# Performance work log

Hardware: AMD Instinct MI355X
Metric: run time of the kernel (lower is better)

The kernel has to match this reference:

```python
import jax, jax.numpy as jnp
import numpy as np

L, N, D = 4, 50000, 64        # lookback, n_nodes, gnn_dim
E = 500000                    # n_edges
HID = 256
LN_EPS = 1e-5


def setup_inputs() -> dict:
    key = jax.random.key(0)
    ks = jax.random.split(key, 8)
    h_all = jax.random.normal(ks[0], (L, N, D), dtype=jnp.float32)
    src = jax.random.randint(ks[1], (E,), 0, N, dtype=jnp.int32)
    dst = jax.random.randint(ks[2], (E,), 0, N, dtype=jnp.int32)
    W1 = jax.random.normal(ks[3], (HID, L * 2 * D), dtype=jnp.float32) * (1.0 / np.sqrt(L * 2 * D))
    b1 = jax.random.normal(ks[4], (HID,), dtype=jnp.float32) * 0.01
    W3 = jax.random.normal(ks[5], (1, HID), dtype=jnp.float32) * (1.0 / np.sqrt(HID))
    b3 = jax.random.normal(ks[6], (1,), dtype=jnp.float32) * 0.01
    gamma2 = jnp.ones((HID,), dtype=jnp.float32)
    beta2 = jnp.zeros((HID,), dtype=jnp.float32)
    return {"h_all": h_all, "src": src, "dst": dst, "W1": W1, "b1": b1,
            "W3": W3, "b3": b3, "gamma2": gamma2, "beta2": beta2}


def reference(h_all, src, dst, W1, b1, W3, b3, gamma2, beta2):
    lb, _, d = h_all.shape
    # importance weights 1..L normalized
    imp = jnp.arange(1, lb + 1, dtype=h_all.dtype)
    imp = imp / imp.sum()
    # per-edge gather of src/dst features for every lookback step: [L, E, 2D]
    hs = h_all[:, src]                                  # [L, E, D]
    hd = h_all[:, dst]                                  # [L, E, D]
    embed = jnp.concatenate([hs, hd], axis=-1) * imp[:, None, None]
    # concat over lookback steps -> [E, L*2D]
    embed = jnp.transpose(embed, (1, 0, 2)).reshape(embed.shape[1], -1)
    # MLP: W1(tanh) -> LayerNorm -> dropout(eval=identity) -> relu -> W3
    x = jnp.tanh(embed) @ W1.T + b1                     # [E, HID]
    mu = jnp.mean(x, axis=-1, keepdims=True)
    var = jnp.var(x, axis=-1, keepdims=True)
    x = (x - mu) * jax.lax.rsqrt(var + LN_EPS) * gamma2 + beta2
    x = jax.nn.relu(x)
    out = x @ W3.T + b3                                 # [E, 1]
    return out[:, 0]
```

## Files before the change

kernel.cpp:

```cpp
#include <hip/hip_runtime.h>
#include <hip/hip_bf16.h>

#define LL 4
#define NN 50000
#define DD 64
#define EE 500000
#define HID 256
#define KDIM 512
#define LN_EPS 1e-5f

typedef __bf16 bf16x8 __attribute__((ext_vector_type(8)));
typedef float f32x16 __attribute__((ext_vector_type(16)));

__device__ __forceinline__ void async16(const void* g, void* l) {
    __builtin_amdgcn_global_load_lds(
        (const __attribute__((address_space(1))) void*)g,
        (__attribute__((address_space(3))) void*)l, 16, 0, 0);
}

__global__ void tanh_conv(const float* __restrict__ h, __bf16* __restrict__ t) {
    int i = (blockIdx.x * 256 + threadIdx.x) * 8;
    int l = i / (NN * DD);
    float imp = (float)(l + 1) * 0.1f;
    const float4* p = (const float4*)(h + i);
    float4 a = p[0];
    float4 b = p[1];
    float x[8] = {a.x, a.y, a.z, a.w, b.x, b.y, b.z, b.w};
    bf16x8 r;
    #pragma unroll
    for (int j = 0; j < 8; ++j) {
        float e2 = __expf(2.0f * (imp * x[j]));
        r[j] = (__bf16)(1.0f - 2.0f / (e2 + 1.0f));
    }
    *(bf16x8*)(t + i) = r;
}

__global__ void w2_conv(const float* __restrict__ w1, __bf16* __restrict__ o) {
    int t = blockIdx.x * 256 + threadIdx.x;
    int j  = t & 511;
    int b  = t >> 9;
    int k0 = (b >> 1) * 16 + (b & 1) * 8;
    int r  = j & 255;
    int col = (k0 >> 6) * 128 + ((j >> 8) ? 64 : 0) + (k0 & 63);
    const float4* p = (const float4*)(w1 + r * KDIM + col);
    float4 va = p[0];
    float4 vb = p[1];
    bf16x8 v;
    v[0] = (__bf16)va.x; v[1] = (__bf16)va.y; v[2] = (__bf16)va.z; v[3] = (__bf16)va.w;
    v[4] = (__bf16)vb.x; v[5] = (__bf16)vb.y; v[6] = (__bf16)vb.z; v[7] = (__bf16)vb.w;
    *(bf16x8*)(o + (size_t)t * 8) = v;
}

__global__ __launch_bounds__(256, 2)
void node_proj(const __bf16* __restrict__ tb, const __bf16* __restrict__ w2c,
               const float* __restrict__ b1, __bf16* __restrict__ P) {
    __shared__ __align__(16) char smem[65536];
    __bf16* Bs = (__bf16*)smem;
    float*  Cs = (float*)smem;

    const int tid  = threadIdx.x;
    const int wave = tid >> 6;
    const int lane = tid & 63;
    const int h32  = lane >> 5;
    const int c32  = lane & 31;
    const int cb   = blockIdx.y;
    const int n00  = blockIdx.x * 128;

    #pragma unroll
    for (int it = 0; it < 16; ++it) {
        int o = it * 2048 + tid * 8;
        async16(w2c + (size_t)(o >> 10) * 4096 + cb * 1024 + (o & 1023), Bs + o);
    }

    int node = n00 + wave * 32 + c32;
    if (node >= NN) node = NN - 1;
    uint4 a[16];
    #pragma unroll
    for (int u = 0; u < 16; ++u) {
        const __bf16* p = tb + (size_t)(u >> 2) * (NN * DD) + node * DD
                        + (u & 3) * 16 + h32 * 8;
        a[u] = *(const uint4*)p;
    }

    f32x16 acc[4];
    #pragma unroll
    for (int nt = 0; nt < 4; ++nt) acc[nt] = (f32x16)(0.f);

    __syncthreads();

    #pragma unroll
    for (int u = 0; u < 16; ++u) {
        bf16x8 af = __builtin_bit_cast(bf16x8, a[u]);
        const __bf16* Bk = Bs + (u * 2 + h32) * 1024 + c32 * 8;
        #pragma unroll
        for (int nt = 0; nt < 4; ++nt) {
            bf16x8 bf = *(const bf16x8*)(Bk + nt * 256);
            acc[nt] = __builtin_amdgcn_mfma_f32_32x32x16_bf16(af, bf, acc[nt], 0, 0, 0);
        }
    }
    __syncthreads();

    #pragma unroll
    for (int nt = 0; nt < 4; ++nt) {
        #pragma unroll
        for (int r = 0; r < 16; ++r) {
            int nl = wave * 32 + (r & 3) + 8 * (r >> 2) + 4 * h32;
            Cs[nl * 128 + nt * 32 + c32] = acc[nt][r];
        }
    }
    __syncthreads();
    #pragma unroll
    for (int it = 0; it < 8; ++it) {
        int o  = it * 2048 + tid * 8;
        int nl = o >> 7;
        int n  = n00 + nl;
        if (n < NN) {
            int hbase = ((cb & 1) << 7) | (o & 127);
            bf16x8 v;
            #pragma unroll
            for (int z = 0; z < 8; ++z)
                v[z] = (__bf16)(Cs[o + z] + 0.5f * b1[hbase + z]);
            *(bf16x8*)(P + (size_t)n * 512 + cb * 128 + (o & 127)) = v;
        }
    }
}

__global__ __launch_bounds__(256, 5)
void edge_out(const __bf16* __restrict__ P, const int* __restrict__ src,
              const int* __restrict__ dst, const float* __restrict__ w3,
              const float* __restrict__ b3, const float* __restrict__ gamma,
              const float* __restrict__ beta, float* __restrict__ out) {
    const int tid = threadIdx.x;
    const int g   = tid >> 4;
    const int j   = tid & 15;
    const int lb  = (g & 3) << 4;

    float gv[16], btv[16], wv[16];
    {
        const float4* pg = (const float4*)(gamma + j * 16);
        const float4* pt = (const float4*)(beta + j * 16);
        const float4* pw = (const float4*)(w3 + j * 16);
        #pragma unroll
        for (int z = 0; z < 4; ++z) {
            float4 vg = pg[z], vt = pt[z], vw = pw[z];
            gv [z*4+0] = vg.x; gv [z*4+1] = vg.y; gv [z*4+2] = vg.z; gv [z*4+3] = vg.w;
            btv[z*4+0] = vt.x; btv[z*4+1] = vt.y; btv[z*4+2] = vt.z; btv[z*4+3] = vt.w;
            wv [z*4+0] = vw.x; wv [z*4+1] = vw.y; wv [z*4+2] = vw.z; wv [z*4+3] = vw.w;
        }
    }
    const float b3v = b3[0];
    const int e0 = blockIdx.x * 128 + g * 8;

    int ej = e0 + (j & 7);
    if (ej >= EE) ej = EE - 1;
    const int sv = src[ej];
    const int dv = dst[ej];

    #pragma unroll
    for (int i = 0; i < 8; ++i) {
        const int s = __shfl(sv, lb + i);
        const int d = __shfl(dv, lb + i);
        const uint4* ps = (const uint4*)(P + ((size_t)s << 9) + (j << 4));
        const uint4* pd = (const uint4*)(P + ((size_t)d << 9) + 256 + (j << 4));
        uint4 rs0 = ps[0], rs1 = ps[1];
        uint4 rd0 = pd[0], rd1 = pd[1];
        bf16x8 A0 = __builtin_bit_cast(bf16x8, rs0);
        bf16x8 A1 = __builtin_bit_cast(bf16x8, rs1);
        bf16x8 C0 = __builtin_bit_cast(bf16x8, rd0);
        bf16x8 C1 = __builtin_bit_cast(bf16x8, rd1);
        float x[16];
        #pragma unroll
        for (int z = 0; z < 8; ++z) {
            x[z]     = (float)A0[z] + (float)C0[z];
            x[z + 8] = (float)A1[z] + (float)C1[z];
        }
        float sum = 0.f, sq = 0.f;
        #pragma unroll
        for (int z = 0; z < 16; ++z) {
            sum += x[z];
            sq   = fmaf(x[z], x[z], sq);
        }
        #pragma unroll
        for (int m = 1; m < 16; m <<= 1) {
            sum += __shfl_xor(sum, m);
            sq  += __shfl_xor(sq,  m);
        }
        float mu = sum * (1.0f / 256.0f);
        float rs = rsqrtf(sq * (1.0f / 256.0f) - mu * mu + LN_EPS);
        float dot = 0.f;
        #pragma unroll
        for (int z = 0; z < 16; ++z) {
            float t = (x[z] - mu) * rs;
            float y = fmaxf(fmaf(t, gv[z], btv[z]), 0.f);
            dot = fmaf(y, wv[z], dot);
        }
        #pragma unroll
        for (int m = 1; m < 16; m <<= 1) dot += __shfl_xor(dot, m);
        int e = e0 + i;
        if (j == 0 && e < EE) out[e] = dot + b3v;
    }
}

extern "C" void kernel_launch(void* const* d_in, const int* in_sizes, int n_in,
                              void* d_out, int out_size, void* d_ws, size_t ws_size,
                              hipStream_t stream) {
    const float* h_all  = (const float*)d_in[0];
    const int*   src    = (const int*)  d_in[1];
    const int*   dst    = (const int*)  d_in[2];
    const float* W1     = (const float*)d_in[3];
    const float* b1     = (const float*)d_in[4];
    const float* W3     = (const float*)d_in[5];
    const float* b3     = (const float*)d_in[6];
    const float* gamma2 = (const float*)d_in[7];
    const float* beta2  = (const float*)d_in[8];
    float* out = (float*)d_out;

    __bf16* tb  = (__bf16*)d_ws;
    __bf16* w2c = tb + (size_t)LL * NN * DD;
    __bf16* P   = w2c + 131072;

    tanh_conv<<<6250, 256, 0, stream>>>(h_all, tb);
    w2_conv<<<64, 256, 0, stream>>>(W1, w2c);
    node_proj<<<dim3((NN + 127) / 128, 4), 256, 0, stream>>>(tb, w2c, b1, P);
    edge_out<<<(EE + 127) / 128, 256, 0, stream>>>(P, src, dst, W3, b3,
                                                   gamma2, beta2, out);
}
```

Before: 211.3 us.

## Halve node_proj tile width and software-pipeline edge gathers in edge_out

```diff
diff --git a/kernel.cpp b/kernel.cpp
--- a/kernel.cpp
+++ b/kernel.cpp
@@ -51,10 +51,10 @@
     *(bf16x8*)(o + (size_t)t * 8) = v;
 }
 
-__global__ __launch_bounds__(256, 2)
+__global__ __launch_bounds__(256, 4)
 void node_proj(const __bf16* __restrict__ tb, const __bf16* __restrict__ w2c,
                const float* __restrict__ b1, __bf16* __restrict__ P) {
-    __shared__ __align__(16) char smem[65536];
+    __shared__ __align__(16) char smem[32768];
     __bf16* Bs = (__bf16*)smem;
     float*  Cs = (float*)smem;
 
@@ -66,12 +66,6 @@
     const int cb   = blockIdx.y;
     const int n00  = blockIdx.x * 128;
 
-    #pragma unroll
-    for (int it = 0; it < 16; ++it) {
-        int o = it * 2048 + tid * 8;
-        async16(w2c + (size_t)(o >> 10) * 4096 + cb * 1024 + (o & 1023), Bs + o);
-    }
-
     int node = n00 + wave * 32 + c32;
     if (node >= NN) node = NN - 1;
     uint4 a[16];
@@ -82,66 +76,118 @@
         a[u] = *(const uint4*)p;
     }
 
-    f32x16 acc[4];
-    #pragma unroll
-    for (int nt = 0; nt < 4; ++nt) acc[nt] = (f32x16)(0.f);
+    #pragma unroll
+    for (int it = 0; it < 8; ++it) {
+        int o = it * 2048 + tid * 8;
+        async16(w2c + (size_t)(o >> 9) * 4096 + cb * 512 + (o & 511), Bs + o);
+    }
+
+    f32x16 acc[2];
+    acc[0] = (f32x16)(0.f);
+    acc[1] = (f32x16)(0.f);
 
     __syncthreads();
 
     #pragma unroll
     for (int u = 0; u < 16; ++u) {
         bf16x8 af = __builtin_bit_cast(bf16x8, a[u]);
-        const __bf16* Bk = Bs + (u * 2 + h32) * 1024 + c32 * 8;
-        #pragma unroll
-        for (int nt = 0; nt < 4; ++nt) {
-            bf16x8 bf = *(const bf16x8*)(Bk + nt * 256);
-            acc[nt] = __builtin_amdgcn_mfma_f32_32x32x16_bf16(af, bf, acc[nt], 0, 0, 0);
-        }
+        const __bf16* Bk = Bs + (u * 2 + h32) * 512 + c32 * 8;
+        acc[0] = __builtin_amdgcn_mfma_f32_32x32x16_bf16(
+            af, *(const bf16x8*)(Bk), acc[0], 0, 0, 0);
+        acc[1] = __builtin_amdgcn_mfma_f32_32x32x16_bf16(
+            af, *(const bf16x8*)(Bk + 256), acc[1], 0, 0, 0);
     }
     __syncthreads();
 
     #pragma unroll
-    for (int nt = 0; nt < 4; ++nt) {
+    for (int nt = 0; nt < 2; ++nt) {
         #pragma unroll
         for (int r = 0; r < 16; ++r) {
             int nl = wave * 32 + (r & 3) + 8 * (r >> 2) + 4 * h32;
-            Cs[nl * 128 + nt * 32 + c32] = acc[nt][r];
+            Cs[nl * 64 + nt * 32 + c32] = acc[nt][r];
         }
     }
     __syncthreads();
     #pragma unroll
-    for (int it = 0; it < 8; ++it) {
-        int o  = it * 2048 + tid * 8;
-        int nl = o >> 7;
-        int n  = n00 + nl;
+    for (int it = 0; it < 4; ++it) {
+        int o   = it * 2048 + tid * 8;
+        int nl  = o >> 6;
+        int col = o & 63;
+        int n   = n00 + nl;
         if (n < NN) {
-            int hbase = ((cb & 1) << 7) | (o & 127);
+            int hbase = (cb & 3) * 64 + col;
             bf16x8 v;
             #pragma unroll
             for (int z = 0; z < 8; ++z)
                 v[z] = (__bf16)(Cs[o + z] + 0.5f * b1[hbase + z]);
-            *(bf16x8*)(P + (size_t)n * 512 + cb * 128 + (o & 127)) = v;
+            *(bf16x8*)(P + (size_t)n * 512 + cb * 64 + col) = v;
         }
     }
 }
 
-__global__ __launch_bounds__(256, 5)
+#define LOADB(R)                                                              \
+    do {                                                                      \
+        _Pragma("unroll")                                                     \
+        for (int t = 0; t < 4; ++t) {                                         \
+            int s = __shfl(sv, lb + eb + t);                                  \
+            int d = __shfl(dv, lb + eb + t);                                  \
+            R##0[t] = *(const uint4*)(P + ((size_t)s << 9) + (j << 3));       \
+            R##1[t] = *(const uint4*)(P + ((size_t)d << 9) + 256 + (j << 3)); \
+        }                                                                     \
+    } while (0)
+
+#define COMPB(R, B)                                                           \
+    do {                                                                      \
+        _Pragma("unroll")                                                     \
+        for (int t = 0; t < 4; ++t) {                                         \
+            bf16x8 A = __builtin_bit_cast(bf16x8, R##0[t]);                   \
+            bf16x8 C = __builtin_bit_cast(bf16x8, R##1[t]);                   \
+            float x[8];                                                       \
+            _Pragma("unroll")                                                 \
+            for (int z = 0; z < 8; ++z) x[z] = (float)A[z] + (float)C[z];     \
+            float sum = 0.f, sq = 0.f;                                        \
+            _Pragma("unroll")                                                 \
+            for (int z = 0; z < 8; ++z) {                                     \
+                sum += x[z];                                                  \
+                sq   = fmaf(x[z], x[z], sq);                                  \
+            }                                                                 \
+            _Pragma("unroll")                                                 \
+            for (int m = 1; m < 32; m <<= 1) {                                \
+                sum += __shfl_xor(sum, m);                                    \
+                sq  += __shfl_xor(sq,  m);                                    \
+            }                                                                 \
+            float mu = sum * (1.0f / 256.0f);                                 \
+            float rs = rsqrtf(sq * (1.0f / 256.0f) - mu * mu + LN_EPS);       \
+            float dot = 0.f;                                                  \
+            _Pragma("unroll")                                                 \
+            for (int z = 0; z < 8; ++z) {                                     \
+                float y = fmaxf(fmaf((x[z] - mu) * rs, gv[z], btv[z]), 0.f);  \
+                dot = fmaf(y, wv[z], dot);                                    \
+            }                                                                 \
+            _Pragma("unroll")                                                 \
+            for (int m = 1; m < 32; m <<= 1) dot += __shfl_xor(dot, m);       \
+            int e = e0 + (B) * 4 + t;                                         \
+            if (j == 0 && e < EE) out[e] = dot + b3v;                         \
+        }                                                                     \
+    } while (0)
+
+__global__ __launch_bounds__(256, 4)
 void edge_out(const __bf16* __restrict__ P, const int* __restrict__ src,
               const int* __restrict__ dst, const float* __restrict__ w3,
               const float* __restrict__ b3, const float* __restrict__ gamma,
               const float* __restrict__ beta, float* __restrict__ out) {
     const int tid = threadIdx.x;
-    const int g   = tid >> 4;
-    const int j   = tid & 15;
-    const int lb  = (g & 3) << 4;
-
-    float gv[16], btv[16], wv[16];
-    {
-        const float4* pg = (const float4*)(gamma + j * 16);
-        const float4* pt = (const float4*)(beta + j * 16);
-        const float4* pw = (const float4*)(w3 + j * 16);
+    const int g   = tid >> 5;
+    const int j   = tid & 31;
+    const int lb  = (g & 1) << 5;
+
+    float gv[8], btv[8], wv[8];
+    {
+        const float4* pg = (const float4*)(gamma + j * 8);
+        const float4* pt = (const float4*)(beta + j * 8);
+        const float4* pw = (const float4*)(w3 + j * 8);
         #pragma unroll
-        for (int z = 0; z < 4; ++z) {
+        for (int z = 0; z < 2; ++z) {
             float4 vg = pg[z], vt = pt[z], vw = pw[z];
             gv [z*4+0] = vg.x; gv [z*4+1] = vg.y; gv [z*4+2] = vg.z; gv [z*4+3] = vg.w;
             btv[z*4+0] = vt.x; btv[z*4+1] = vt.y; btv[z*4+2] = vt.z; btv[z*4+3] = vt.w;
@@ -149,56 +195,34 @@
         }
     }
     const float b3v = b3[0];
-    const int e0 = blockIdx.x * 128 + g * 8;
-
-    int ej = e0 + (j & 7);
+    const int e0 = blockIdx.x * 128 + g * 16;
+
+    int ej = e0 + (j & 15);
     if (ej >= EE) ej = EE - 1;
     const int sv = src[ej];
     const int dv = dst[ej];
 
-    #pragma unroll
-    for (int i = 0; i < 8; ++i) {
-        const int s = __shfl(sv, lb + i);
-        const int d = __shfl(dv, lb + i);
-        const uint4* ps = (const uint4*)(P + ((size_t)s << 9) + (j << 4));
-        const uint4* pd = (const uint4*)(P + ((size_t)d << 9) + 256 + (j << 4));
-        uint4 rs0 = ps[0], rs1 = ps[1];
-        uint4 rd0 = pd[0], rd1 = pd[1];
-        bf16x8 A0 = __builtin_bit_cast(bf16x8, rs0);
-        bf16x8 A1 = __builtin_bit_cast(bf16x8, rs1);
-        bf16x8 C0 = __builtin_bit_cast(bf16x8, rd0);
-        bf16x8 C1 = __builtin_bit_cast(bf16x8, rd1);
-        float x[16];
-        #pragma unroll
-        for (int z = 0; z < 8; ++z) {
-            x[z]     = (float)A0[z] + (float)C0[z];
-            x[z + 8] = (float)A1[z] + (float)C1[z];
-        }
-        float sum = 0.f, sq = 0.f;
-        #pragma unroll
-        for (int z = 0; z < 16; ++z) {
-            sum += x[z];
-            sq   = fmaf(x[z], x[z], sq);
-        }
-        #pragma unroll
-        for (int m = 1; m < 16; m <<= 1) {
-            sum += __shfl_xor(sum, m);
-            sq  += __shfl_xor(sq,  m);
-        }
-        float mu = sum * (1.0f / 256.0f);
-        float rs = rsqrtf(sq * (1.0f / 256.0f) - mu * mu + LN_EPS);
-        float dot = 0.f;
-        #pragma unroll
-        for (int z = 0; z < 16; ++z) {
-            float t = (x[z] - mu) * rs;
-            float y = fmaxf(fmaf(t, gv[z], btv[z]), 0.f);
-            dot = fmaf(y, wv[z], dot);
-        }
-        #pragma unroll
-        for (int m = 1; m < 16; m <<= 1) dot += __shfl_xor(dot, m);
-        int e = e0 + i;
-        if (j == 0 && e < EE) out[e] = dot + b3v;
-    }
+    uint4 ra0[4], ra1[4], rb0[4], rb1[4];
+    {
+        const int eb = 0;
+        LOADB(ra);
+    }
+    {
+        const int eb = 4;
+        LOADB(rb);
+    }
+    {
+        const int eb = 8;
+        COMPB(ra, 0);
+        LOADB(ra);
+    }
+    {
+        const int eb = 12;
+        COMPB(rb, 1);
+        LOADB(rb);
+    }
+    COMPB(ra, 2);
+    COMPB(rb, 3);
 }
 
 extern "C" void kernel_launch(void* const* d_in, const int* in_sizes, int n_in,
@@ -221,7 +245,7 @@
 
     tanh_conv<<<6250, 256, 0, stream>>>(h_all, tb);
     w2_conv<<<64, 256, 0, stream>>>(W1, w2c);
-    node_proj<<<dim3((NN + 127) / 128, 4), 256, 0, stream>>>(tb, w2c, b1, P);
+    node_proj<<<dim3((NN + 127) / 128, 8), 256, 0, stream>>>(tb, w2c, b1, P);
     edge_out<<<(EE + 127) / 128, 256, 0, stream>>>(P, src, dst, W3, b3,
                                                    gamma2, beta2, out);
 }
```

Result: no change. 213.6 us (+1.1%).

## Fuse tanh conversion into node projection and software-pipeline edge gathers

Applied to the files above, without the earlier changes.

```diff
diff --git a/kernel.cpp b/kernel.cpp
--- a/kernel.cpp
+++ b/kernel.cpp
@@ -16,23 +16,6 @@
     __builtin_amdgcn_global_load_lds(
         (const __attribute__((address_space(1))) void*)g,
         (__attribute__((address_space(3))) void*)l, 16, 0, 0);
-}
-
-__global__ void tanh_conv(const float* __restrict__ h, __bf16* __restrict__ t) {
-    int i = (blockIdx.x * 256 + threadIdx.x) * 8;
-    int l = i / (NN * DD);
-    float imp = (float)(l + 1) * 0.1f;
-    const float4* p = (const float4*)(h + i);
-    float4 a = p[0];
-    float4 b = p[1];
-    float x[8] = {a.x, a.y, a.z, a.w, b.x, b.y, b.z, b.w};
-    bf16x8 r;
-    #pragma unroll
-    for (int j = 0; j < 8; ++j) {
-        float e2 = __expf(2.0f * (imp * x[j]));
-        r[j] = (__bf16)(1.0f - 2.0f / (e2 + 1.0f));
-    }
-    *(bf16x8*)(t + i) = r;
 }
 
 __global__ void w2_conv(const float* __restrict__ w1, __bf16* __restrict__ o) {
@@ -52,7 +35,7 @@
 }
 
 __global__ __launch_bounds__(256, 2)
-void node_proj(const __bf16* __restrict__ tb, const __bf16* __restrict__ w2c,
+void node_proj(const float* __restrict__ h_all, const __bf16* __restrict__ w2c,
                const float* __restrict__ b1, __bf16* __restrict__ P) {
     __shared__ __align__(16) char smem[65536];
     __bf16* Bs = (__bf16*)smem;
@@ -63,69 +46,95 @@
     const int lane = tid & 63;
     const int h32  = lane >> 5;
     const int c32  = lane & 31;
-    const int cb   = blockIdx.y;
     const int n00  = blockIdx.x * 128;
-
-    #pragma unroll
-    for (int it = 0; it < 16; ++it) {
-        int o = it * 2048 + tid * 8;
-        async16(w2c + (size_t)(o >> 10) * 4096 + cb * 1024 + (o & 1023), Bs + o);
-    }
 
     int node = n00 + wave * 32 + c32;
     if (node >= NN) node = NN - 1;
-    uint4 a[16];
+
+    bf16x8 a[16];
     #pragma unroll
-    for (int u = 0; u < 16; ++u) {
-        const __bf16* p = tb + (size_t)(u >> 2) * (NN * DD) + node * DD
-                        + (u & 3) * 16 + h32 * 8;
-        a[u] = *(const uint4*)p;
-    }
-
-    f32x16 acc[4];
+    for (int uh = 0; uh < 2; ++uh) {
+        float4 f[16];
+        #pragma unroll
+        for (int u8 = 0; u8 < 8; ++u8) {
+            int u = uh * 8 + u8;
+            const float* p = h_all + ((size_t)(u >> 2) * NN + node) * DD
+                           + (u & 3) * 16 + h32 * 8;
+            f[u8 * 2]     = *(const float4*)p;
+            f[u8 * 2 + 1] = *(const float4*)(p + 4);
+        }
+        #pragma unroll
+        for (int u8 = 0; u8 < 8; ++u8) {
+            int u = uh * 8 + u8;
+            float imp = (float)((u >> 2) + 1) * 0.1f;
+            float xs[8] = {f[u8*2].x, f[u8*2].y, f[u8*2].z, f[u8*2].w,
+                           f[u8*2+1].x, f[u8*2+1].y, f[u8*2+1].z, f[u8*2+1].w};
+            bf16x8 r;
+            #pragma unroll
+            for (int z = 0; z < 8; ++z) {
+                float e2 = __expf(2.0f * (imp * xs[z]));
+                r[z] = (__bf16)(1.0f - 2.0f / (e2 + 1.0f));
+            }
+            a[u] = r;
+        }
+    }
+
     #pragma unroll
-    for (int nt = 0; nt < 4; ++nt) acc[nt] = (f32x16)(0.f);
-
-    __syncthreads();
-
-    #pragma unroll
-    for (int u = 0; u < 16; ++u) {
-        bf16x8 af = __builtin_bit_cast(bf16x8, a[u]);
-        const __bf16* Bk = Bs + (u * 2 + h32) * 1024 + c32 * 8;
+    for (int cbi = 0; cbi < 2; ++cbi) {
+        const int cc = blockIdx.y * 2 + cbi;
+
+        #pragma unroll
+        for (int it = 0; it < 16; ++it) {
+            int o = it * 2048 + tid * 8;
+            async16(w2c + (size_t)(o >> 10) * 4096 + cc * 1024 + (o & 1023), Bs + o);
+        }
+
+        f32x16 acc[4];
+        #pragma unroll
+        for (int nt = 0; nt < 4; ++nt) acc[nt] = (f32x16)(0.f);
+
+        __syncthreads();
+
+        #pragma unroll
+        for (int u = 0; u < 16; ++u) {
+            const __bf16* Bk = Bs + (u * 2 + h32) * 1024 + c32 * 8;
+            #pragma unroll
+            for (int nt = 0; nt < 4; ++nt) {
+                bf16x8 bf = *(const bf16x8*)(Bk + nt * 256);
+                acc[nt] = __builtin_amdgcn_mfma_f32_32x32x16_bf16(a[u], bf, acc[nt], 0, 0, 0);
+            }
+        }
+        __syncthreads();
+
         #pragma unroll
         for (int nt = 0; nt < 4; ++nt) {
-            bf16x8 bf = *(const bf16x8*)(Bk + nt * 256);
-            acc[nt] = __builtin_amdgcn_mfma_f32_32x32x16_bf16(af, bf, acc[nt], 0, 0, 0);
-        }
-    }
-    __syncthreads();
-
-    #pragma unroll
-    for (int nt = 0; nt < 4; ++nt) {
-        #pragma unroll
-        for (int r = 0; r < 16; ++r) {
-            int nl = wave * 32 + (r & 3) + 8 * (r >> 2) + 4 * h32;
-            Cs[nl * 128 + nt * 32 + c32] = acc[nt][r];
-        }
-    }
-    __syncthreads();
-    #pragma unroll
-    for (int it = 0; it < 8; ++it) {
-        int o  = it * 2048 + tid * 8;
-        int nl = o >> 7;
-        int n  = n00 + nl;
-        if (n < NN) {
-            int hbase = ((cb & 1) << 7) | (o & 127);
-            bf16x8 v;
             #pragma unroll
-            for (int z = 0; z < 8; ++z)
-                v[z] = (__bf16)(Cs[o + z] + 0.5f * b1[hbase + z]);
-            *(bf16x8*)(P + (size_t)n * 512 + cb * 128 + (o & 127)) = v;
-        }
-    }
-}
-
-__global__ __launch_bounds__(256, 5)
+            for (int r = 0; r < 16; ++r) {
+                int nl = wave * 32 + (r & 3) + 8 * (r >> 2) + 4 * h32;
+                Cs[nl * 128 + nt * 32 + c32] = acc[nt][r];
+            }
+        }
+        __syncthreads();
+        #pragma unroll
+        for (int it = 0; it < 8; ++it) {
+            int o   = it * 2048 + tid * 8;
+            int nl  = o >> 7;
+            int col = o & 127;
+            int n   = n00 + nl;
+            if (n < NN) {
+                int hb = ((cc & 1) << 7) | col;
+                bf16x8 v;
+                #pragma unroll
+                for (int z = 0; z < 8; ++z)
+                    v[z] = (__bf16)(Cs[o + z] + 0.5f * b1[hb + z]);
+                *(bf16x8*)(P + (size_t)n * 512 + cc * 128 + col) = v;
+            }
+        }
+        __syncthreads();
+    }
+}
+
+__global__ __launch_bounds__(256, 4)
 void edge_out(const __bf16* __restrict__ P, const int* __restrict__ src,
               const int* __restrict__ dst, const float* __restrict__ w3,
               const float* __restrict__ b3, const float* __restrict__ gamma,
@@ -133,7 +142,6 @@
     const int tid = threadIdx.x;
     const int g   = tid >> 4;
     const int j   = tid & 15;
-    const int lb  = (g & 3) << 4;
 
     float gv[16], btv[16], wv[16];
     {
@@ -151,23 +159,28 @@
     const float b3v = b3[0];
     const int e0 = blockIdx.x * 128 + g * 8;
 
-    int ej = e0 + (j & 7);
-    if (ej >= EE) ej = EE - 1;
-    const int sv = src[ej];
-    const int dv = dst[ej];
-
+    uint4 cs0, cs1, cd0, cd1, ns0, ns1, nd0, nd1;
+    {
+        int ec = e0 < EE ? e0 : EE - 1;
+        int s = src[ec], d = dst[ec];
+        const uint4* ps = (const uint4*)(P + ((size_t)s << 9) + (j << 4));
+        const uint4* pd = (const uint4*)(P + ((size_t)d << 9) + 256 + (j << 4));
+        cs0 = ps[0]; cs1 = ps[1]; cd0 = pd[0]; cd1 = pd[1];
+    }
     #pragma unroll
     for (int i = 0; i < 8; ++i) {
-        const int s = __shfl(sv, lb + i);
-        const int d = __shfl(dv, lb + i);
-        const uint4* ps = (const uint4*)(P + ((size_t)s << 9) + (j << 4));
-        const uint4* pd = (const uint4*)(P + ((size_t)d << 9) + 256 + (j << 4));
-        uint4 rs0 = ps[0], rs1 = ps[1];
-        uint4 rd0 = pd[0], rd1 = pd[1];
-        bf16x8 A0 = __builtin_bit_cast(bf16x8, rs0);
-        bf16x8 A1 = __builtin_bit_cast(bf16x8, rs1);
-        bf16x8 C0 = __builtin_bit_cast(bf16x8, rd0);
-        bf16x8 C1 = __builtin_bit_cast(bf16x8, rd1);
+        if (i < 7) {
+            int e = e0 + i + 1;
+            int ec = e < EE ? e : EE - 1;
+            int s = src[ec], d = dst[ec];
+            const uint4* ps = (const uint4*)(P + ((size_t)s << 9) + (j << 4));
+            const uint4* pd = (const uint4*)(P + ((size_t)d << 9) + 256 + (j << 4));
+            ns0 = ps[0]; ns1 = ps[1]; nd0 = pd[0]; nd1 = pd[1];
+        }
+        bf16x8 A0 = __builtin_bit_cast(bf16x8, cs0);
+        bf16x8 A1 = __builtin_bit_cast(bf16x8, cs1);
+        bf16x8 C0 = __builtin_bit_cast(bf16x8, cd0);
+        bf16x8 C1 = __builtin_bit_cast(bf16x8, cd1);
         float x[16];
         #pragma unroll
         for (int z = 0; z < 8; ++z) {
@@ -190,14 +203,14 @@
         float dot = 0.f;
         #pragma unroll
         for (int z = 0; z < 16; ++z) {
-            float t = (x[z] - mu) * rs;
-            float y = fmaxf(fmaf(t, gv[z], btv[z]), 0.f);
+            float y = fmaxf(fmaf((x[z] - mu) * rs, gv[z], btv[z]), 0.f);
             dot = fmaf(y, wv[z], dot);
         }
         #pragma unroll
         for (int m = 1; m < 16; m <<= 1) dot += __shfl_xor(dot, m);
         int e = e0 + i;
         if (j == 0 && e < EE) out[e] = dot + b3v;
+        cs0 = ns0; cs1 = ns1; cd0 = nd0; cd1 = nd1;
     }
 }
 
@@ -215,13 +228,11 @@
     const float* beta2  = (const float*)d_in[8];
     float* out = (float*)d_out;
 
-    __bf16* tb  = (__bf16*)d_ws;
-    __bf16* w2c = tb + (size_t)LL * NN * DD;
+    __bf16* w2c = (__bf16*)d_ws;
     __bf16* P   = w2c + 131072;
 
-    tanh_conv<<<6250, 256, 0, stream>>>(h_all, tb);
     w2_conv<<<64, 256, 0, stream>>>(W1, w2c);
-    node_proj<<<dim3((NN + 127) / 128, 4), 256, 0, stream>>>(tb, w2c, b1, P);
+    node_proj<<<dim3((NN + 127) / 128, 2), 256, 0, stream>>>(h_all, w2c, b1, P);
     edge_out<<<(EE + 127) / 128, 256, 0, stream>>>(P, src, dst, W3, b3,
                                                    gamma2, beta2, out);
 }
```

New measurement: 204.9 us. 1.03x faster.
